# Kernel tuning notes

Measured on AMD Instinct MI355X. Metric: run time of the kernel, lower is better.

Reference implementation:

```python
import jax, jax.numpy as jnp
import numpy as np

B, S, N, FI = 16, 96, 128, 1
H_LSTM, NLAYERS = 128, 3
COMB = H_LSTM + 16 * N  # 128 + 16*128 = 2176


def setup_inputs() -> dict:
    key = jax.random.key(0)
    ks = list(jax.random.split(key, 24))
    def nrm(k, shape, scale=0.1):
        return jax.random.normal(k, shape, dtype=jnp.float32) * scale
    x = jax.random.normal(ks[0], (B, S, N, FI), dtype=jnp.float32)
    adj = jax.random.randint(ks[1], (N, N), 0, 2).astype(jnp.float32)
    adj = jnp.maximum(adj, jnp.eye(N, dtype=jnp.float32))  # self-loops so no row fully masked
    return {
        "x": x, "adj": adj,
        "W_emb": nrm(ks[2], (1, 32)), "b_emb": jnp.zeros((32,), jnp.float32),
        "W1": nrm(ks[3], (32, 32)), "a1": nrm(ks[4], (64,)),
        "W2": nrm(ks[5], (32, 16)), "a2": nrm(ks[6], (32,)),
        "lstm_Wih": nrm(ks[7], (NLAYERS, 4 * H_LSTM, N)),
        "lstm_Whh": nrm(ks[8], (NLAYERS, 4 * H_LSTM, H_LSTM)),
        "lstm_bih": jnp.zeros((NLAYERS, 4 * H_LSTM), jnp.float32),
        "lstm_bhh": jnp.zeros((NLAYERS, 4 * H_LSTM), jnp.float32),
        "head_W1": nrm(ks[9], (3, COMB, 64), 0.05), "head_b1": jnp.zeros((3, 64), jnp.float32),
        "head_W2": nrm(ks[10], (3, 64, 32)), "head_b2": jnp.zeros((3, 32), jnp.float32),
        "W3d": nrm(ks[11], (32, 1)), "b3d": jnp.zeros((1,), jnp.float32),
        "W3r": nrm(ks[12], (32, 1)), "b3r": jnp.zeros((1,), jnp.float32),
        "W3v": nrm(ks[13], (32, 2)), "b3v": jnp.zeros((2,), jnp.float32),
    }


def gat(h, adj, W, a, apply_elu):
    # h: [M, N, Fin]; equivalent to concat-matmul score: e_ij = leakyrelu(a_l.Wh_i + a_r.Wh_j)
    Wh = h @ W                      # [M, N, Fout]
    f = W.shape[1]
    left = Wh @ a[:f]               # [M, N]
    right = Wh @ a[f:]              # [M, N]
    e = jax.nn.leaky_relu(left[:, :, None] + right[:, None, :], 0.2)  # [M, N, N]
    e = jnp.where(adj[None, :, :] > 0, e, jnp.float32(-9e15))
    attn = jax.nn.softmax(e, axis=2)
    out = jnp.einsum('mij,mjf->mif', attn, Wh)
    return (jax.nn.elu(out) if apply_elu else out), attn


def _lstm_layer(seq, Wih, Whh, bih, bhh):
    # seq: [B, S, D]; PyTorch gate order i, f, g, o
    Bz, Hh = seq.shape[0], Whh.shape[1]
    b = bih + bhh
    def step(carry, xt):
        h, c = carry
        g = xt @ Wih.T + h @ Whh.T + b  # [B, 4H]
        i, f, gg, o = jnp.split(g, 4, axis=1)
        c = jax.nn.sigmoid(f) * c + jax.nn.sigmoid(i) * jnp.tanh(gg)
        h = jax.nn.sigmoid(o) * jnp.tanh(c)
        return (h, c), h
    init = (jnp.zeros((Bz, Hh), seq.dtype), jnp.zeros((Bz, Hh), seq.dtype))
    _, hs = jax.lax.scan(step, init, jnp.swapaxes(seq, 0, 1))
    return jnp.swapaxes(hs, 0, 1)


def lstm_forward(seq, Wih, Whh, bih, bhh):
    h = seq
    for l in range(Wih.shape[0]):  # 3 layers (inference: inter-layer dropout is identity)
        h = _lstm_layer(h, Wih[l], Whh[l], bih[l], bhh[l])
    return h


def reference(x, adj, W_emb, b_emb, W1, a1, W2, a2,
              lstm_Wih, lstm_Whh, lstm_bih, lstm_bhh,
              head_W1, head_b1, head_W2, head_b2,
              W3d, b3d, W3r, b3r, W3v, b3v):
    Bz, Sz, Nz, _ = x.shape
    x_emb = (x @ W_emb + b_emb).reshape(Bz * Sz, Nz, -1)  # [B*S, N, 32]
    xg, _ = gat(x_emb, adj, W1, a1, True)
    xg, attn2 = gat(xg, adj, W2, a2, False)
    xg_out = xg.reshape(Bz, Sz, -1)[:, -1, :]             # [B, 16*N]
    xl = lstm_forward(x.reshape(Bz, Sz, Nz), lstm_Wih, lstm_Whh, lstm_bih, lstm_bhh)
    xl_out = xl[:, -1, :]                                 # [B, 128]
    c = jnp.concatenate([xl_out, xg_out], axis=1)         # [B, COMB]
    h1 = jax.nn.relu(jnp.einsum('bc,kcd->kbd', c, head_W1) + head_b1[:, None, :])
    h2 = jax.nn.relu(jnp.einsum('kbd,kde->kbe', h1, head_W2) + head_b2[:, None, :])
    d = h2[0] @ W3d + b3d
    r = h2[1] @ W3r + b3r
    v = h2[2] @ W3v + b3v
    return (d, r, v, attn2)
```

## Files before the change

### kernel.cpp

```cpp
#include <hip/hip_runtime.h>
#include <hip/hip_bf16.h>


typedef _Float16 half8 __attribute__((ext_vector_type(8)));
typedef float floatx4 __attribute__((ext_vector_type(4)));
typedef float float4v __attribute__((ext_vector_type(4)));

#define LOG2E 1.44269504088896f

__device__ __forceinline__ float fast_exp(float x) {
    return __builtin_amdgcn_exp2f(x * LOG2E);
}
__device__ __forceinline__ float sigm(float x) {
    x = fminf(fmaxf(x, -30.f), 30.f);
    return __builtin_amdgcn_rcpf(1.f + __builtin_amdgcn_exp2f(-x * LOG2E));
}
__device__ __forceinline__ float tanhp(float x) {
    x = fminf(fmaxf(x, -15.f), 15.f);
    float e = __builtin_amdgcn_exp2f(-2.f * LOG2E * x);
    return (1.f - e) * __builtin_amdgcn_rcpf(1.f + e);
}
__device__ __forceinline__ void split8v(float4v v0, float4v v1, half8& hi, half8& lo) {
#pragma unroll
    for (int j = 0; j < 4; ++j) {
        _Float16 h = (_Float16)v0[j];
        hi[j] = h; lo[j] = (_Float16)(v0[j] - (float)h);
    }
#pragma unroll
    for (int j = 0; j < 4; ++j) {
        _Float16 h = (_Float16)v1[j];
        hi[4 + j] = h; lo[4 + j] = (_Float16)(v1[j] - (float)h);
    }
}

struct LstmSh {
    float hbuf[2][544];
    float stage[16 * 132];
};
struct GatSh {
    unsigned long long adjm[256];
    float xv[128];
    float u1[32], v1[32], coef[4];
    float s1v[128];
    float h2s[128 * 33];
    float wh2[128 * 17];
    float Lv[128], Rv[128], rd2[128];
    float d_h[4][128], s_h[4][128];
};
union ShU { LstmSh l; GatSh g; };

__device__ __forceinline__ void l0_body(LstmSh& sh, int b,
    const float* __restrict__ x, const float* __restrict__ Wih,
    const float* __restrict__ Whh, const float* __restrict__ bih,
    const float* __restrict__ bhh,
    float* __restrict__ Pre0,
    float* __restrict__ Hout,
    int* __restrict__ fHout)
{
    int tid = threadIdx.x;
    int w = tid >> 6, lane = tid & 63, quad = lane >> 4, sub = lane & 15;
    int hu = 16 * w + sub, c4 = quad;

    __builtin_amdgcn_s_setprio(1);
    {
        half8 bhi[4][4], blo[4][4];
        float bias[4];
#pragma unroll
        for (int tt = 0; tt < 4; ++tt) {
            int r = tt * 128 + 16 * w + sub;
            bias[tt] = bih[r] + bhh[r];
#pragma unroll
            for (int kc = 0; kc < 4; ++kc) {
                const float4v* p = (const float4v*)(Wih + r * 128 + kc * 32 + quad * 8);
                split8v(p[0], p[1], bhi[tt][kc], blo[tt][kc]);
            }
        }
        for (int mt = 0; mt < 6; ++mt) {
            half8 ahi[4], alo[4];
            const float* arow = x + b * 12288 + (mt * 16 + sub) * 128;
#pragma unroll
            for (int kc = 0; kc < 4; ++kc) {
                const float4v* p = (const float4v*)(arow + kc * 32 + quad * 8);
                split8v(p[0], p[1], ahi[kc], alo[kc]);
            }
            floatx4 acc[4];
#pragma unroll
            for (int tt = 0; tt < 4; ++tt) {
                floatx4 a = {bias[tt], bias[tt], bias[tt], bias[tt]};
                acc[tt] = a;
            }
#pragma unroll
            for (int tt = 0; tt < 4; ++tt)
#pragma unroll
                for (int kc = 0; kc < 4; ++kc) {
                    acc[tt] = __builtin_amdgcn_mfma_f32_16x16x32_f16(ahi[kc], bhi[tt][kc], acc[tt], 0, 0, 0);
                    acc[tt] = __builtin_amdgcn_mfma_f32_16x16x32_f16(ahi[kc], blo[tt][kc], acc[tt], 0, 0, 0);
                    acc[tt] = __builtin_amdgcn_mfma_f32_16x16x32_f16(alo[kc], bhi[tt][kc], acc[tt], 0, 0, 0);
                }
#pragma unroll
            for (int tt = 0; tt < 4; ++tt)
#pragma unroll
                for (int reg = 0; reg < 4; ++reg)
                    Pre0[(mt * 16 + quad * 4 + reg) * 512 + tt * 128 + 16 * w + sub] = acc[tt][reg];
        }
    }
    float4v wgt[4][8];
#pragma unroll
    for (int g = 0; g < 4; ++g) {
        const float4v* p = (const float4v*)(Whh + (g * 128 + hu) * 128 + c4 * 32);
#pragma unroll
        for (int k = 0; k < 8; ++k) wgt[g][k] = p[k];
    }
    sh.hbuf[0][c4 * 136 + hu] = 0.f;
    float cvar = 0.f;
    __syncthreads();

    for (int t = 0; t < 96; ++t) {
        int rb = t & 1, wb = rb ^ 1;
        float pre[4];
#pragma unroll
        for (int g = 0; g < 4; ++g)
            pre[g] = Pre0[t * 512 + g * 128 + hu];
        const float4v* hc = (const float4v*)(&sh.hbuf[rb][c4 * 168]);
        float4v p4[4];
#pragma unroll
        for (int g = 0; g < 4; ++g) { float4v z = {0.f,0.f,0.f,0.f}; p4[g] = z; }
#pragma unroll
        for (int k = 0; k < 8; ++k) {
            float4v hv = hc[k];
#pragma unroll
            for (int g = 0; g < 4; ++g) p4[g] += wgt[g][k] * hv;
        }
        float p[4];
#pragma unroll
        for (int g = 0; g < 4; ++g) {
            float s = p4[g].x + p4[g].y + p4[g].z + p4[g].w;
            s += __shfl_xor(s, 16, 64);
            s += __shfl_xor(s, 32, 64);
            p[g] = s + pre[g];
        }
        float c = sigm(p[1]) * cvar + sigm(p[0]) * tanhp(p[2]);
        cvar = c;
        float h = sigm(p[3]) * tanhp(c);
        sh.hbuf[wb][c4 * 136 + hu] = h;
        if (c4 == 0) sh.stage[(t & 15) * 132 + hu] = h;
        __syncthreads();
        if ((t & 15) == 15) {
            int k = t >> 4;
            float* outp = Hout + k * 2048;
#pragma unroll
            for (int u = 0; u < 4; ++u) {
                int e = tid * 4 + u;
                atomicExch(&outp[e], sh.stage[(e >> 7) * 132 + (e & 127)]);
            }
            __syncthreads();
            if (tid == 0) atomicExch(&fHout[k], 1);
        }
    }
    __builtin_amdgcn_s_setprio(0);
}

__device__ __forceinline__ void proj_body(LstmSh& sh, int layer,
    const float* __restrict__ Wih, const float* __restrict__ bih,
    const float* __restrict__ bhh,
    const float* __restrict__ Hin,
    int* __restrict__ fH,
    float* __restrict__ PreRing,
    int* __restrict__ fP,
    int* __restrict__ cons)
{
    int tid = threadIdx.x;
    int w = tid >> 6, lane = tid & 63, quad = lane >> 4, sub = lane & 15;
    const float* WihL = Wih + layer * 65536;

    half8 bhi[4][4], blo[4][4];
    float bias[4];
#pragma unroll
    for (int tt = 0; tt < 4; ++tt) {
        int r = tt * 128 + 16 * w + sub;
        bias[tt] = bih[layer * 512 + r] + bhh[layer * 512 + r];
#pragma unroll
        for (int kc = 0; kc < 4; ++kc) {
            const float4v* p = (const float4v*)(WihL + r * 128 + kc * 32 + quad * 8);
            split8v(p[0], p[1], bhi[tt][kc], blo[tt][kc]);
        }
    }
    for (int k = 0; k < 6; ++k) {
        if (tid == 0) {
            while (atomicAdd(&fH[k], 0) == 0) __builtin_amdgcn_s_sleep(16);
        }
        __syncthreads();
        {
            const float* inp = Hin + k * 2048;
#pragma unroll
            for (int u = 0; u < 4; ++u) {
                int e = tid * 4 + u;
                sh.stage[(e >> 7) * 132 + (e & 127)] =
                    atomicAdd((float*)&inp[e], 0.f);
            }
        }
        __syncthreads();
        half8 ahi[4], alo[4];
        const float* arow = &sh.stage[sub * 132];
#pragma unroll
        for (int kc = 0; kc < 4; ++kc) {
            const float4v* p = (const float4v*)(arow + kc * 32 + quad * 8);
            split8v(p[0], p[1], ahi[kc], alo[kc]);
        }
        floatx4 acc[4];
#pragma unroll
        for (int tt = 0; tt < 4; ++tt) {
            floatx4 a = {bias[tt], bias[tt], bias[tt], bias[tt]};
            acc[tt] = a;
        }
#pragma unroll
        for (int tt = 0; tt < 4; ++tt)
#pragma unroll
            for (int kc = 0; kc < 4; ++kc) {
                acc[tt] = __builtin_amdgcn_mfma_f32_16x16x32_f16(ahi[kc], bhi[tt][kc], acc[tt], 0, 0, 0);
                acc[tt] = __builtin_amdgcn_mfma_f32_16x16x32_f16(ahi[kc], blo[tt][kc], acc[tt], 0, 0, 0);
                acc[tt] = __builtin_amdgcn_mfma_f32_16x16x32_f16(alo[kc], bhi[tt][kc], acc[tt], 0, 0, 0);
            }
        if (k >= 3) {
            if (tid == 0) {
                while (atomicAdd(cons, 0) < k - 2) __builtin_amdgcn_s_sleep(16);
            }
            __syncthreads();
        }
        float* dst = PreRing + (k % 3) * 8192;
#pragma unroll
        for (int tt = 0; tt < 4; ++tt)
#pragma unroll
            for (int reg = 0; reg < 4; ++reg)
                dst[(quad * 4 + reg) * 512 + tt * 128 + 16 * w + sub] = acc[tt][reg];
        __syncthreads();
        if (tid == 0) {
            __threadfence();
            atomicExch(&fP[k], 1);
        }
    }
}

__device__ __forceinline__ void rec_body(LstmSh& sh, int b, int layer,
    const float* __restrict__ Whh,
    const float* __restrict__ PreRing, int* __restrict__ fP,
    int* __restrict__ cons,
    float* __restrict__ Hout, int* __restrict__ fHout,
    float* __restrict__ xl_out)
{
    int tid = threadIdx.x;
    int w = tid >> 6, lane = tid & 63, quad = lane >> 4, sub = lane & 15;
    int hu = 16 * w + sub, c4 = quad;
    const float* WhhL = Whh + layer * 65536;

    __builtin_amdgcn_s_setprio(1);
    float4v wgt[4][8];
#pragma unroll
    for (int g = 0; g < 4; ++g) {
        const float4v* p = (const float4v*)(WhhL + (g * 128 + hu) * 128 + c4 * 32);
#pragma unroll
        for (int k = 0; k < 8; ++k) wgt[g][k] = p[k];
    }
    sh.hbuf[0][c4 * 136 + hu] = 0.f;
    float cvar = 0.f;
    __syncthreads();

    for (int k = 0; k < 6; ++k) {
        if (tid == 0) {
            while (atomicAdd(&fP[k], 0) == 0) __builtin_amdgcn_s_sleep(16);
            __threadfence();
        }
        __syncthreads();
        const float* PreC = PreRing + (k % 3) * 8192;
        for (int tl = 0; tl < 16; ++tl) {
            int t = k * 16 + tl;
            int rb = t & 1, wb = rb ^ 1;
            float pre[4];
#pragma unroll
            for (int g = 0; g < 4; ++g)
                pre[g] = PreC[tl * 512 + g * 128 + hu];
            const float4v* hc = (const float4v*)(&sh.hbuf[rb][c4 * 168]);
            float4v p4[4];
#pragma unroll
            for (int g = 0; g < 4; ++g) { float4v z = {0.f,0.f,0.f,0.f}; p4[g] = z; }
#pragma unroll
            for (int kk = 0; kk < 8; ++kk) {
                float4v hv = hc[kk];
#pragma unroll
                for (int g = 0; g < 4; ++g) p4[g] += wgt[g][kk] * hv;
            }
            float p[4];
#pragma unroll
            for (int g = 0; g < 4; ++g) {
                float s = p4[g].x + p4[g].y + p4[g].z + p4[g].w;
                s += __shfl_xor(s, 16, 64);
                s += __shfl_xor(s, 32, 64);
                p[g] = s + pre[g];
            }
            float c = sigm(p[1]) * cvar + sigm(p[0]) * tanhp(p[2]);
            cvar = c;
            float h = sigm(p[3]) * tanhp(c);
            sh.hbuf[wb][c4 * 136 + hu] = h;
            if (c4 == 0) {
                if (layer == 1) sh.stage[tl * 132 + hu] = h;
                else if (t == 95) xl_out[b * 128 + hu] = h;
            }
            __syncthreads();
        }
        if (tid == 0) atomicExch(cons, k + 1);
        if (layer == 1) {
            float* outp = Hout + k * 2048;
#pragma unroll
            for (int u = 0; u < 4; ++u) {
                int e = tid * 4 + u;
                atomicExch(&outp[e], sh.stage[(e >> 7) * 132 + (e & 127)]);
            }
            __syncthreads();
            if (tid == 0) atomicExch(&fHout[k], 1);
        }
    }
    __builtin_amdgcn_s_setprio(0);
}

__device__ __forceinline__ void gat_body(GatSh& s, int m,
    const float* __restrict__ x, const float* __restrict__ adj,
    const float* __restrict__ W_emb, const float* __restrict__ b_emb,
    const float* __restrict__ W1, const float* __restrict__ a1,
    const float* __restrict__ W2, const float* __restrict__ a2,
    float* __restrict__ attn_out, float* __restrict__ xg)
{
    int tid = threadIdx.x;

    if (tid < 128) s.xv[tid] = x[m * 128 + tid];
#pragma unroll
    for (int base = 0; base < 16384; base += 512) {
        int idx = base + tid;
        unsigned long long msk = __ballot(adj[idx] > 0.f);
        if ((tid & 63) == 0) s.adjm[idx >> 6] = msk;
    }
    if (tid < 32) {
        float su = 0.f, sv = 0.f;
        for (int kk = 0; kk < 32; ++kk) {
            float w1v = W1[kk * 32 + tid];
            su += W_emb[kk] * w1v;
            sv += b_emb[kk] * w1v;
        }
        s.u1[tid] = su; s.v1[tid] = sv;
    }
    __syncthreads();
    if (tid < 4) {
        const float* av = a1 + ((tid >= 2) ? 32 : 0);
        const float* uv = (tid & 1) ? s.v1 : s.u1;
        float sum = 0.f;
        for (int f = 0; f < 32; ++f) sum += uv[f] * av[f];
        s.coef[tid] = sum;
    }
    __syncthreads();
    float cL = s.coef[0], dL = s.coef[1], cR = s.coef[2], dR = s.coef[3];

    {
        int i = tid & 127, q = tid >> 7;
        unsigned int ms = (unsigned int)(s.adjm[(i << 1) | (q >> 1)] >> ((q & 1) * 32));
        float Li = s.xv[i] * cL + dL;
        float den = 0.f, wsum = 0.f;
        int j0 = q * 32;
#pragma unroll
        for (int jj = 0; jj < 32; ++jj) {
            if ((ms >> jj) & 1) {
                float xj = s.xv[j0 + jj];
                float e = Li + xj * cR + dR;
                e = e > 0.f ? e : 0.2f * e;
                float p = fast_exp(e);
                den += p; wsum += p * xj;
            }
        }
        s.d_h[q][i] = den; s.s_h[q][i] = wsum;
    }
    __syncthreads();
    if (tid < 128) {
        float den = 0.f, wsum = 0.f;
#pragma unroll
        for (int q = 0; q < 4; ++q) { den += s.d_h[q][tid]; wsum += s.s_h[q][tid]; }
        s.s1v[tid] = wsum / den;
    }
    __syncthreads();
#pragma unroll
    for (int e0 = 0; e0 < 4096; e0 += 512) {
        int e = e0 + tid;
        int i = e >> 5, f = e & 31;
        float v = s.s1v[i] * s.u1[f] + s.v1[f];
        s.h2s[i * 33 + f] = v > 0.f ? v : fast_exp(v) - 1.f;
    }
    __syncthreads();
    {
        int i = tid >> 2, g0 = (tid & 3) * 4;
        float accv[4] = {0.f, 0.f, 0.f, 0.f};
        for (int f = 0; f < 32; ++f) {
            float hv = s.h2s[i * 33 + f];
#pragma unroll
            for (int g = 0; g < 4; ++g) accv[g] += hv * W2[f * 16 + g0 + g];
        }
#pragma unroll
        for (int g = 0; g < 4; ++g) s.wh2[i * 17 + g0 + g] = accv[g];
    }
    __syncthreads();
    if (tid < 256) {
        int i = tid & 127, which = tid >> 7;
        const float* aa = a2 + which * 16;
        float sum = 0.f;
#pragma unroll
        for (int g = 0; g < 16; ++g) sum += s.wh2[i * 17 + g] * aa[g];
        (which ? s.Rv : s.Lv)[i] = sum;
    }
    __syncthreads();
    {
        int i = tid & 127, q = tid >> 7;
        unsigned int ms = (unsigned int)(s.adjm[(i << 1) | (q >> 1)] >> ((q & 1) * 32));
        float Li = s.Lv[i];
        float den = 0.f;
        int j0 = q * 32;
#pragma unroll
        for (int jj = 0; jj < 32; ++jj) {
            if ((ms >> jj) & 1) {
                float e = Li + s.Rv[j0 + jj];
                e = e > 0.f ? e : 0.2f * e;
                den += fast_exp(e);
            }
        }
        s.d_h[q][i] = den;
    }
    __syncthreads();
    if (tid < 128) {
        float den = 0.f;
#pragma unroll
        for (int q = 0; q < 4; ++q) den += s.d_h[q][tid];
        s.rd2[tid] = 1.0f / den;
    }
    __syncthreads();

    float* aout = attn_out + (size_t)m * 16384;
#pragma unroll
    for (int k = 0; k < 8; ++k) {
        int e0 = k * 2048 + tid * 4;
        int i = e0 >> 7, j0 = e0 & 127;
        unsigned int bits = (unsigned int)(s.adjm[(i << 1) | (j0 >> 6)] >> (j0 & 63)) & 0xFu;
        float Li = s.Lv[i], ri = s.rd2[i];
        float4v p;
#pragma unroll
        for (int u = 0; u < 4; ++u) {
            float pv = 0.f;
            if ((bits >> u) & 1) {
                float e = Li + s.Rv[j0 + u];
                e = e > 0.f ? e : 0.2f * e;
                pv = fast_exp(e) * ri;
            }
            p[u] = pv;
        }
        *(float4v*)(aout + e0) = p;
    }

    if (m % 96 == 95) {
        int b = m / 96;
        int i = tid >> 2, g0 = (tid & 3) * 4;
        unsigned long long mA = s.adjm[i << 1], mB = s.adjm[(i << 1) | 1];
        float Li = s.Lv[i], ri = s.rd2[i];
        float accv[4] = {0.f, 0.f, 0.f, 0.f};
        for (int j = 0; j < 128; ++j) {
            unsigned long long mm = (j < 64) ? mA : mB;
            if ((mm >> (j & 63)) & 1) {
                float e = Li + s.Rv[j];
                e = e > 0.f ? e : 0.2f * e;
                float p = fast_exp(e) * ri;
#pragma unroll
                for (int g = 0; g < 4; ++g) accv[g] += p * s.wh2[j * 17 + g0 + g];
            }
        }
#pragma unroll
        for (int g = 0; g < 4; ++g) xg[b * 2048 + i * 16 + g0 + g] = accv[g];
    }
}

__global__ __launch_bounds__(512, 2) void fused_kernel(
    const float* __restrict__ x, const float* __restrict__ adj,
    const float* __restrict__ W_emb, const float* __restrict__ b_emb,
    const float* __restrict__ W1, const float* __restrict__ a1,
    const float* __restrict__ W2, const float* __restrict__ a2,
    const float* __restrict__ Wih, const float* __restrict__ Whh,
    const float* __restrict__ bih, const float* __restrict__ bhh,
    float* __restrict__ Pre0, float* __restrict__ Pre1, float* __restrict__ Pre2,
    float* __restrict__ H0, float* __restrict__ H1,
    int* __restrict__ flags, float* __restrict__ xl_out,
    float* __restrict__ attn_out, float* __restrict__ xg)
{
    __shared__ ShU sh;
    int bb = blockIdx.x;
    if (bb < 80) {
        int grp = bb >> 4, b = bb & 15;
        int* F = flags + b * 32;
        if (grp == 0) {
            l0_body(sh.l, b, x, Wih, Whh, bih, bhh,
                    Pre0 + b * 49152, H0 + b * 12288, F + 0);
        } else if (grp == 1) {
            proj_body(sh.l, 1, Wih, bih, bhh,
                      H0 + b * 12288, F + 0, Pre1 + b * 24576, F + 8, F + 14);
        } else if (grp == 2) {
            rec_body(sh.l, b, 1, Whh,
                     Pre1 + b * 24576, F + 8, F + 14,
                     H1 + b * 12288, F + 16, nullptr);
        } else if (grp == 3) {
            proj_body(sh.l, 2, Wih, bih, bhh,
                      H1 + b * 12288, F + 16, Pre2 + b * 24576, F + 24, F + 30);
        } else {
            rec_body(sh.l, b, 2, Whh,
                     Pre2 + b * 24576, F + 24, F + 30,
                     nullptr, nullptr, xl_out);
        }
    } else {
        gat_body(sh.g, bb - 80, x, adj, W_emb, b_emb, W1, a1, W2, a2, attn_out, xg);
    }
}

__global__ __launch_bounds__(256) void head_partial_kernel(
    const float* __restrict__ xl, const float* __restrict__ xg,
    const float* __restrict__ W1, float* __restrict__ hp)
{
    int k = blockIdx.x >> 4, chunk = blockIdx.x & 15;
    int d = threadIdx.x & 63, bg = threadIdx.x >> 6;
    float acc[4] = {0.f, 0.f, 0.f, 0.f};
    int c0 = chunk * 136;
    for (int cc = c0; cc < c0 + 136; ++cc) {
        float wv = W1[(k * 2176 + cc) * 64 + d];
#pragma unroll
        for (int u = 0; u < 4; ++u) {
            int b = bg * 4 + u;
            float cv = (cc < 128) ? xl[b * 128 + cc] : xg[b * 2048 + cc - 128];
            acc[u] += wv * cv;
        }
    }
#pragma unroll
    for (int u = 0; u < 4; ++u)
        hp[(((k * 16 + chunk) * 16) + bg * 4 + u) * 64 + d] = acc[u];
}

__global__ __launch_bounds__(256) void head_final_kernel(
    const float* __restrict__ hp, const float* __restrict__ b1,
    const float* __restrict__ W2, const float* __restrict__ b2,
    const float* __restrict__ W3d, const float* __restrict__ b3d,
    const float* __restrict__ W3r, const float* __restrict__ b3r,
    const float* __restrict__ W3v, const float* __restrict__ b3v,
    float* __restrict__ out)
{
    __shared__ float h1s[3 * 16 * 64];
    __shared__ float h2s[3 * 16 * 32];
    int tid = threadIdx.x;
    for (int o = tid; o < 3072; o += 256) {
        int k = o >> 10, rem = o & 1023, b = rem >> 6, d = rem & 63;
        float s = b1[k * 64 + d];
        for (int ch = 0; ch < 16; ++ch)
            s += hp[(((k * 16 + ch) * 16) + b) * 64 + d];
        h1s[o] = fmaxf(s, 0.f);
    }
    __syncthreads();
    for (int o = tid; o < 1536; o += 256) {
        int k = o >> 9, rem = o & 511, b = rem >> 5, e = rem & 31;
        float s = b2[k * 32 + e];
        for (int dd = 0; dd < 64; ++dd)
            s += h1s[(k * 16 + b) * 64 + dd] * W2[(k * 64 + dd) * 32 + e];
        h2s[o] = fmaxf(s, 0.f);
    }
    __syncthreads();
    if (tid < 64) {
        if (tid < 16) {
            int b = tid; float s = b3d[0];
            for (int e = 0; e < 32; ++e) s += h2s[b * 32 + e] * W3d[e];
            out[b] = s;
        } else if (tid < 32) {
            int b = tid - 16; float s = b3r[0];
            for (int e = 0; e < 32; ++e) s += h2s[(16 + b) * 32 + e] * W3r[e];
            out[16 + b] = s;
        } else {
            int b = (tid - 32) >> 1, j = tid & 1; float s = b3v[j];
            for (int e = 0; e < 32; ++e) s += h2s[(32 + b) * 32 + e] * W3v[e * 2 + j];
            out[32 + b * 2 + j] = s;
        }
    }
}

extern "C" void kernel_launch(void* const* d_in, const int* in_sizes, int n_in,
                              void* d_out, int out_size, void* d_ws, size_t ws_size,
                              hipStream_t stream)
{
    const float* x     = (const float*)d_in[0];
    const float* adj   = (const float*)d_in[1];
    const float* W_emb = (const float*)d_in[2];
    const float* b_emb = (const float*)d_in[3];
    const float* W1    = (const float*)d_in[4];
    const float* a1    = (const float*)d_in[5];
    const float* W2    = (const float*)d_in[6];
    const float* a2    = (const float*)d_in[7];
    const float* Wih   = (const float*)d_in[8];
    const float* Whh   = (const float*)d_in[9];
    const float* bih   = (const float*)d_in[10];
    const float* bhh   = (const float*)d_in[11];
    const float* hW1   = (const float*)d_in[12];
    const float* hb1   = (const float*)d_in[13];
    const float* hW2   = (const float*)d_in[14];
    const float* hb2   = (const float*)d_in[15];
    const float* W3d   = (const float*)d_in[16];
    const float* b3d   = (const float*)d_in[17];
    const float* W3r   = (const float*)d_in[18];
    const float* b3r   = (const float*)d_in[19];
    const float* W3v   = (const float*)d_in[20];
    const float* b3v   = (const float*)d_in[21];

    float* out = (float*)d_out;
    float* wsf = (float*)d_ws;
    float* XG    = wsf;
    float* XL    = wsf + 32768;
    float* HP    = wsf + 34816;
    int*   FLAGS = (int*)(wsf + 83968);
    float* PRE0  = wsf + 84992;
    float* PRE1  = wsf + 871424;
    float* PRE2  = wsf + 1264640;
    float* H0    = wsf + 1657856;
    float* H1    = wsf + 1854464;

    hipMemsetAsync(FLAGS, 0, 16 * 32 * sizeof(int), stream);
    fused_kernel<<<1616, 512, 0, stream>>>(
        x, adj, W_emb, b_emb, W1, a1, W2, a2,
        Wih, Whh, bih, bhh, PRE0, PRE1, PRE2, H0, H1, FLAGS, XL, out + 64, XG);
    head_partial_kernel<<<48, 256, 0, stream>>>(XL, XG, hW1, HP);
    head_final_kernel<<<1, 256, 0, stream>>>(HP, hb1, hW2, hb2, W3d, b3d, W3r, b3r, W3v, b3v, out);
}
```

Before: 353.1 us.

## Double-buffer layer-0 staging, tighten spin sleeps, fuse head kernels via last-block counter

Layer-0 recurrence now double-buffers its output stage so it no longer needs an extra barrier before raising the chunk flag; each flag is raised one step later, and the last one after the loop. Spin-wait sleeps drop from 16 to 2 and the projection workers get raised wave priority. The two head kernels merge into one launch where the last block to finish, found through an atomic counter, does the reduction and the final layers. This trims launch overhead and handoff latency along the LSTM pipeline, at the cost of more polling traffic and a one-step delay on the layer-0 flags.

```diff
diff --git a/kernel.cpp b/kernel.cpp
--- a/kernel.cpp
+++ b/kernel.cpp
@@ -35,7 +35,7 @@
 
 struct LstmSh {
     float hbuf[2][544];
-    float stage[16 * 132];
+    float stage[2][16 * 132];
 };
 struct GatSh {
     unsigned long long adjm[256];
@@ -143,36 +143,38 @@
         cvar = c;
         float h = sigm(p[3]) * tanhp(c);
         sh.hbuf[wb][c4 * 136 + hu] = h;
-        if (c4 == 0) sh.stage[(t & 15) * 132 + hu] = h;
+        if (c4 == 0) sh.stage[(t >> 4) & 1][(t & 15) * 132 + hu] = h;
         __syncthreads();
         if ((t & 15) == 15) {
             int k = t >> 4;
             float* outp = Hout + k * 2048;
+            const float* st = sh.stage[k & 1];
 #pragma unroll
             for (int u = 0; u < 4; ++u) {
                 int e = tid * 4 + u;
-                atomicExch(&outp[e], sh.stage[(e >> 7) * 132 + (e & 127)]);
-            }
-            __syncthreads();
-            if (tid == 0) atomicExch(&fHout[k], 1);
-        }
-    }
+                atomicExch(&outp[e], st[(e >> 7) * 132 + (e & 127)]);
+            }
+        } else if ((t & 15) == 0 && t >= 16 && tid == 0) {
+            atomicExch(&fHout[(t >> 4) - 1], 1);
+        }
+    }
+    __syncthreads();
+    if (tid == 0) atomicExch(&fHout[5], 1);
     __builtin_amdgcn_s_setprio(0);
 }
 
 __device__ __forceinline__ void proj_body(LstmSh& sh, int layer,
     const float* __restrict__ Wih, const float* __restrict__ bih,
     const float* __restrict__ bhh,
-    const float* __restrict__ Hin,
-    int* __restrict__ fH,
-    float* __restrict__ PreRing,
-    int* __restrict__ fP,
+    const float* __restrict__ Hin, int* __restrict__ fH,
+    float* __restrict__ PreRing, int* __restrict__ fP,
     int* __restrict__ cons)
 {
     int tid = threadIdx.x;
     int w = tid >> 6, lane = tid & 63, quad = lane >> 4, sub = lane & 15;
     const float* WihL = Wih + layer * 65536;
 
+    __builtin_amdgcn_s_setprio(1);
     half8 bhi[4][4], blo[4][4];
     float bias[4];
 #pragma unroll
@@ -187,7 +189,7 @@
     }
     for (int k = 0; k < 6; ++k) {
         if (tid == 0) {
-            while (atomicAdd(&fH[k], 0) == 0) __builtin_amdgcn_s_sleep(16);
+            while (atomicAdd(&fH[k], 0) == 0) __builtin_amdgcn_s_sleep(2);
         }
         __syncthreads();
         {
@@ -195,13 +197,13 @@
 #pragma unroll
             for (int u = 0; u < 4; ++u) {
                 int e = tid * 4 + u;
-                sh.stage[(e >> 7) * 132 + (e & 127)] =
+                sh.stage[0][(e >> 7) * 132 + (e & 127)] =
                     atomicAdd((float*)&inp[e], 0.f);
             }
         }
         __syncthreads();
         half8 ahi[4], alo[4];
-        const float* arow = &sh.stage[sub * 132];
+        const float* arow = &sh.stage[0][sub * 132];
 #pragma unroll
         for (int kc = 0; kc < 4; ++kc) {
             const float4v* p = (const float4v*)(arow + kc * 32 + quad * 8);
@@ -223,7 +225,7 @@
             }
         if (k >= 3) {
             if (tid == 0) {
-                while (atomicAdd(cons, 0) < k - 2) __builtin_amdgcn_s_sleep(16);
+                while (atomicAdd(cons, 0) < k - 2) __builtin_amdgcn_s_sleep(2);
             }
             __syncthreads();
         }
@@ -239,6 +241,7 @@
             atomicExch(&fP[k], 1);
         }
     }
+    __builtin_amdgcn_s_setprio(0);
 }
 
 __device__ __forceinline__ void rec_body(LstmSh& sh, int b, int layer,
@@ -267,7 +270,7 @@
 
     for (int k = 0; k < 6; ++k) {
         if (tid == 0) {
-            while (atomicAdd(&fP[k], 0) == 0) __builtin_amdgcn_s_sleep(16);
+            while (atomicAdd(&fP[k], 0) == 0) __builtin_amdgcn_s_sleep(2);
             __threadfence();
         }
         __syncthreads();
@@ -302,7 +305,7 @@
             float h = sigm(p[3]) * tanhp(c);
             sh.hbuf[wb][c4 * 136 + hu] = h;
             if (c4 == 0) {
-                if (layer == 1) sh.stage[tl * 132 + hu] = h;
+                if (layer == 1) sh.stage[0][tl * 132 + hu] = h;
                 else if (t == 95) xl_out[b * 128 + hu] = h;
             }
             __syncthreads();
@@ -313,7 +316,7 @@
 #pragma unroll
             for (int u = 0; u < 4; ++u) {
                 int e = tid * 4 + u;
-                atomicExch(&outp[e], sh.stage[(e >> 7) * 132 + (e & 127)]);
+                atomicExch(&outp[e], sh.stage[0][(e >> 7) * 132 + (e & 127)]);
             }
             __syncthreads();
             if (tid == 0) atomicExch(&fHout[k], 1);
@@ -520,30 +523,11 @@
     }
 }
 
-__global__ __launch_bounds__(256) void head_partial_kernel(
+__global__ __launch_bounds__(256) void head_kernel(
     const float* __restrict__ xl, const float* __restrict__ xg,
-    const float* __restrict__ W1, float* __restrict__ hp)
-{
-    int k = blockIdx.x >> 4, chunk = blockIdx.x & 15;
-    int d = threadIdx.x & 63, bg = threadIdx.x >> 6;
-    float acc[4] = {0.f, 0.f, 0.f, 0.f};
-    int c0 = chunk * 136;
-    for (int cc = c0; cc < c0 + 136; ++cc) {
-        float wv = W1[(k * 2176 + cc) * 64 + d];
-#pragma unroll
-        for (int u = 0; u < 4; ++u) {
-            int b = bg * 4 + u;
-            float cv = (cc < 128) ? xl[b * 128 + cc] : xg[b * 2048 + cc - 128];
-            acc[u] += wv * cv;
-        }
-    }
-#pragma unroll
-    for (int u = 0; u < 4; ++u)
-        hp[(((k * 16 + chunk) * 16) + bg * 4 + u) * 64 + d] = acc[u];
-}
-
-__global__ __launch_bounds__(256) void head_final_kernel(
-    const float* __restrict__ hp, const float* __restrict__ b1,
+    const float* __restrict__ W1, float* __restrict__ hp,
+    int* __restrict__ counter,
+    const float* __restrict__ b1,
     const float* __restrict__ W2, const float* __restrict__ b2,
     const float* __restrict__ W3d, const float* __restrict__ b3d,
     const float* __restrict__ W3r, const float* __restrict__ b3r,
@@ -552,7 +536,35 @@
 {
     __shared__ float h1s[3 * 16 * 64];
     __shared__ float h2s[3 * 16 * 32];
+    __shared__ int isLast;
     int tid = threadIdx.x;
+    {
+        int k = blockIdx.x >> 4, chunk = blockIdx.x & 15;
+        int d = tid & 63, bg = tid >> 6;
+        float acc[4] = {0.f, 0.f, 0.f, 0.f};
+        int c0 = chunk * 136;
+        for (int cc = c0; cc < c0 + 136; ++cc) {
+            float wv = W1[(k * 2176 + cc) * 64 + d];
+#pragma unroll
+            for (int u = 0; u < 4; ++u) {
+                int b = bg * 4 + u;
+                float cv = (cc < 128) ? xl[b * 128 + cc] : xg[b * 2048 + cc - 128];
+                acc[u] += wv * cv;
+            }
+        }
+#pragma unroll
+        for (int u = 0; u < 4; ++u)
+            hp[(((k * 16 + chunk) * 16) + bg * 4 + u) * 64 + d] = acc[u];
+    }
+    __threadfence();
+    if (tid == 0) {
+        int old = atomicAdd(counter, 1);
+        isLast = (old == 47);
+    }
+    __syncthreads();
+    if (!isLast) return;
+    __threadfence();
+
     for (int o = tid; o < 3072; o += 256) {
         int k = o >> 10, rem = o & 1023, b = rem >> 6, d = rem & 63;
         float s = b1[k * 64 + d];
@@ -625,10 +637,11 @@
     float* H0    = wsf + 1657856;
     float* H1    = wsf + 1854464;
 
-    hipMemsetAsync(FLAGS, 0, 16 * 32 * sizeof(int), stream);
+    hipMemsetAsync(FLAGS, 0, (16 * 32 + 8) * sizeof(int), stream);
     fused_kernel<<<1616, 512, 0, stream>>>(
         x, adj, W_emb, b_emb, W1, a1, W2, a2,
         Wih, Whh, bih, bhh, PRE0, PRE1, PRE2, H0, H1, FLAGS, XL, out + 64, XG);
-    head_partial_kernel<<<48, 256, 0, stream>>>(XL, XG, hW1, HP);
-    head_final_kernel<<<1, 256, 0, stream>>>(HP, hb1, hW2, hb2, W3d, b3d, W3r, b3r, W3v, b3v, out);
-}
+    head_kernel<<<48, 256, 0, stream>>>(
+        XL, XG, hW1, HP, FLAGS + 512,
+        hb1, hW2, hb2, W3d, b3d, W3r, b3r, W3v, b3v, out);
+}
```

Result: slower. 360.9 us (+2.2%).

## Batch LSTM recurrence across all sequences into one MFMA block per layer

Applied to the files above, without the earlier changes.

Replaces the per-batch-element recurrent blocks (16 per layer, scalar FMA dot products with shuffles) with a single block per layer that handles all 16 batch rows together. It computes h@Whh^T with split-fp16 MFMA and stores preactivations in a batch-interleaved layout. Projection blocks now run per batch element and signal per-(chunk, batch) flags, and layer 0 gets a separate projection stage. Spin-wait sleeps are shortened and launch bounds drop to one block per SM. The serial chain now depends on one block and 16-way flag polling, and the lower occupancy may slow the concurrent GAT blocks.

```diff
diff --git a/kernel.cpp b/kernel.cpp
--- a/kernel.cpp
+++ b/kernel.cpp
@@ -33,11 +33,14 @@
     }
 }
 
-struct LstmSh {
-    float hbuf[2][544];
+struct __align__(16) MegaSh {
+    float g[512 * 20];
+    float h[16 * 132];
+};
+struct __align__(16) ProjSh {
     float stage[16 * 132];
 };
-struct GatSh {
+struct __align__(16) GatSh {
     unsigned long long adjm[256];
     float xv[128];
     float u1[32], v1[32], coef[4];
@@ -47,132 +50,79 @@
     float Lv[128], Rv[128], rd2[128];
     float d_h[4][128], s_h[4][128];
 };
-union ShU { LstmSh l; GatSh g; };
-
-__device__ __forceinline__ void l0_body(LstmSh& sh, int b,
+union ShU { MegaSh m; ProjSh p; GatSh gt; };
+
+__device__ __forceinline__ void l0proj_body(int b,
     const float* __restrict__ x, const float* __restrict__ Wih,
-    const float* __restrict__ Whh, const float* __restrict__ bih,
-    const float* __restrict__ bhh,
-    float* __restrict__ Pre0,
-    float* __restrict__ Hout,
-    int* __restrict__ fHout)
+    const float* __restrict__ bih, const float* __restrict__ bhh,
+    float* __restrict__ PreM0, int* __restrict__ fL0)
 {
     int tid = threadIdx.x;
     int w = tid >> 6, lane = tid & 63, quad = lane >> 4, sub = lane & 15;
-    int hu = 16 * w + sub, c4 = quad;
 
     __builtin_amdgcn_s_setprio(1);
-    {
-        half8 bhi[4][4], blo[4][4];
-        float bias[4];
+    half8 bhi[4][4], blo[4][4];
+    float bias[4];
+#pragma unroll
+    for (int tt = 0; tt < 4; ++tt) {
+        int r = tt * 128 + 16 * w + sub;
+        bias[tt] = bih[r] + bhh[r];
+#pragma unroll
+        for (int kc = 0; kc < 4; ++kc) {
+            const float4v* p = (const float4v*)(Wih + r * 128 + kc * 32 + quad * 8);
+            split8v(p[0], p[1], bhi[tt][kc], blo[tt][kc]);
+        }
+    }
+    for (int mt = 0; mt < 6; ++mt) {
+        half8 ahi[4], alo[4];
+        const float* arow = x + b * 12288 + (mt * 16 + sub) * 128;
+#pragma unroll
+        for (int kc = 0; kc < 4; ++kc) {
+            const float4v* p = (const float4v*)(arow + kc * 32 + quad * 8);
+            split8v(p[0], p[1], ahi[kc], alo[kc]);
+        }
+        floatx4 acc[4];
 #pragma unroll
         for (int tt = 0; tt < 4; ++tt) {
-            int r = tt * 128 + 16 * w + sub;
-            bias[tt] = bih[r] + bhh[r];
+            floatx4 a = {bias[tt], bias[tt], bias[tt], bias[tt]};
+            acc[tt] = a;
+        }
+#pragma unroll
+        for (int tt = 0; tt < 4; ++tt)
 #pragma unroll
             for (int kc = 0; kc < 4; ++kc) {
-                const float4v* p = (const float4v*)(Wih + r * 128 + kc * 32 + quad * 8);
-                split8v(p[0], p[1], bhi[tt][kc], blo[tt][kc]);
-            }
-        }
-        for (int mt = 0; mt < 6; ++mt) {
-            half8 ahi[4], alo[4];
-            const float* arow = x + b * 12288 + (mt * 16 + sub) * 128;
-#pragma unroll
-            for (int kc = 0; kc < 4; ++kc) {
-                const float4v* p = (const float4v*)(arow + kc * 32 + quad * 8);
-                split8v(p[0], p[1], ahi[kc], alo[kc]);
-            }
-            floatx4 acc[4];
-#pragma unroll
-            for (int tt = 0; tt < 4; ++tt) {
-                floatx4 a = {bias[tt], bias[tt], bias[tt], bias[tt]};
-                acc[tt] = a;
-            }
-#pragma unroll
-            for (int tt = 0; tt < 4; ++tt)
-#pragma unroll
-                for (int kc = 0; kc < 4; ++kc) {
-                    acc[tt] = __builtin_amdgcn_mfma_f32_16x16x32_f16(ahi[kc], bhi[tt][kc], acc[tt], 0, 0, 0);
-                    acc[tt] = __builtin_amdgcn_mfma_f32_16x16x32_f16(ahi[kc], blo[tt][kc], acc[tt], 0, 0, 0);
-                    acc[tt] = __builtin_amdgcn_mfma_f32_16x16x32_f16(alo[kc], bhi[tt][kc], acc[tt], 0, 0, 0);
-                }
-#pragma unroll
-            for (int tt = 0; tt < 4; ++tt)
-#pragma unroll
-                for (int reg = 0; reg < 4; ++reg)
-                    Pre0[(mt * 16 + quad * 4 + reg) * 512 + tt * 128 + 16 * w + sub] = acc[tt][reg];
-        }
-    }
-    float4v wgt[4][8];
-#pragma unroll
-    for (int g = 0; g < 4; ++g) {
-        const float4v* p = (const float4v*)(Whh + (g * 128 + hu) * 128 + c4 * 32);
-#pragma unroll
-        for (int k = 0; k < 8; ++k) wgt[g][k] = p[k];
-    }
-    sh.hbuf[0][c4 * 136 + hu] = 0.f;
-    float cvar = 0.f;
-    __syncthreads();
-
-    for (int t = 0; t < 96; ++t) {
-        int rb = t & 1, wb = rb ^ 1;
-        float pre[4];
-#pragma unroll
-        for (int g = 0; g < 4; ++g)
-            pre[g] = Pre0[t * 512 + g * 128 + hu];
-        const float4v* hc = (const float4v*)(&sh.hbuf[rb][c4 * 168]);
-        float4v p4[4];
-#pragma unroll
-        for (int g = 0; g < 4; ++g) { float4v z = {0.f,0.f,0.f,0.f}; p4[g] = z; }
-#pragma unroll
-        for (int k = 0; k < 8; ++k) {
-            float4v hv = hc[k];
-#pragma unroll
-            for (int g = 0; g < 4; ++g) p4[g] += wgt[g][k] * hv;
-        }
-        float p[4];
-#pragma unroll
-        for (int g = 0; g < 4; ++g) {
-            float s = p4[g].x + p4[g].y + p4[g].z + p4[g].w;
-            s += __shfl_xor(s, 16, 64);
-            s += __shfl_xor(s, 32, 64);
-            p[g] = s + pre[g];
-        }
-        float c = sigm(p[1]) * cvar + sigm(p[0]) * tanhp(p[2]);
-        cvar = c;
-        float h = sigm(p[3]) * tanhp(c);
-        sh.hbuf[wb][c4 * 136 + hu] = h;
-        if (c4 == 0) sh.stage[(t & 15) * 132 + hu] = h;
+                acc[tt] = __builtin_amdgcn_mfma_f32_16x16x32_f16(ahi[kc], bhi[tt][kc], acc[tt], 0, 0, 0);
+                acc[tt] = __builtin_amdgcn_mfma_f32_16x16x32_f16(ahi[kc], blo[tt][kc], acc[tt], 0, 0, 0);
+                acc[tt] = __builtin_amdgcn_mfma_f32_16x16x32_f16(alo[kc], bhi[tt][kc], acc[tt], 0, 0, 0);
+            }
+#pragma unroll
+        for (int tt = 0; tt < 4; ++tt) {
+            int r2 = tt * 128 + 16 * w + sub;
+#pragma unroll
+            for (int reg = 0; reg < 4; ++reg)
+                PreM0[(((mt * 16 + quad * 4 + reg) * 512) + r2) * 16 + b] = acc[tt][reg];
+        }
         __syncthreads();
-        if ((t & 15) == 15) {
-            int k = t >> 4;
-            float* outp = Hout + k * 2048;
-#pragma unroll
-            for (int u = 0; u < 4; ++u) {
-                int e = tid * 4 + u;
-                atomicExch(&outp[e], sh.stage[(e >> 7) * 132 + (e & 127)]);
-            }
-            __syncthreads();
-            if (tid == 0) atomicExch(&fHout[k], 1);
+        if (tid == 0) {
+            __threadfence();
+            atomicExch(&fL0[b * 8 + mt], 1);
         }
     }
     __builtin_amdgcn_s_setprio(0);
 }
 
-__device__ __forceinline__ void proj_body(LstmSh& sh, int layer,
+__device__ __forceinline__ void proj_body(ProjSh& sh, int layer, int b,
     const float* __restrict__ Wih, const float* __restrict__ bih,
     const float* __restrict__ bhh,
-    const float* __restrict__ Hin,
-    int* __restrict__ fH,
-    float* __restrict__ PreRing,
-    int* __restrict__ fP,
+    const float* __restrict__ Hin, int* __restrict__ fH,
+    float* __restrict__ PreRing, int* __restrict__ fP,
     int* __restrict__ cons)
 {
     int tid = threadIdx.x;
     int w = tid >> 6, lane = tid & 63, quad = lane >> 4, sub = lane & 15;
     const float* WihL = Wih + layer * 65536;
 
+    __builtin_amdgcn_s_setprio(1);
     half8 bhi[4][4], blo[4][4];
     float bias[4];
 #pragma unroll
@@ -187,7 +137,7 @@
     }
     for (int k = 0; k < 6; ++k) {
         if (tid == 0) {
-            while (atomicAdd(&fH[k], 0) == 0) __builtin_amdgcn_s_sleep(16);
+            while (atomicAdd(&fH[k], 0) == 0) __builtin_amdgcn_s_sleep(2);
         }
         __syncthreads();
         {
@@ -223,100 +173,134 @@
             }
         if (k >= 3) {
             if (tid == 0) {
-                while (atomicAdd(cons, 0) < k - 2) __builtin_amdgcn_s_sleep(16);
+                while (atomicAdd(cons, 0) < k - 2) __builtin_amdgcn_s_sleep(2);
             }
             __syncthreads();
         }
-        float* dst = PreRing + (k % 3) * 8192;
-#pragma unroll
-        for (int tt = 0; tt < 4; ++tt)
+        float* dst = PreRing + (k % 3) * 131072;
+#pragma unroll
+        for (int tt = 0; tt < 4; ++tt) {
+            int r2 = tt * 128 + 16 * w + sub;
 #pragma unroll
             for (int reg = 0; reg < 4; ++reg)
-                dst[(quad * 4 + reg) * 512 + tt * 128 + 16 * w + sub] = acc[tt][reg];
+                dst[(((quad * 4 + reg) * 512) + r2) * 16 + b] = acc[tt][reg];
+        }
         __syncthreads();
         if (tid == 0) {
             __threadfence();
-            atomicExch(&fP[k], 1);
-        }
-    }
-}
-
-__device__ __forceinline__ void rec_body(LstmSh& sh, int b, int layer,
-    const float* __restrict__ Whh,
-    const float* __restrict__ PreRing, int* __restrict__ fP,
+            atomicExch(&fP[k * 16 + b], 1);
+        }
+    }
+    __builtin_amdgcn_s_setprio(0);
+}
+
+__device__ __forceinline__ void megarec_body(MegaSh& sh, int layer,
+    const float* __restrict__ WhhL,
+    const float* __restrict__ PreSrc,
+    int* __restrict__ fPre,
     int* __restrict__ cons,
-    float* __restrict__ Hout, int* __restrict__ fHout,
+    float* __restrict__ Hout,
+    int* __restrict__ fHout,
     float* __restrict__ xl_out)
 {
     int tid = threadIdx.x;
     int w = tid >> 6, lane = tid & 63, quad = lane >> 4, sub = lane & 15;
-    int hu = 16 * w + sub, c4 = quad;
-    const float* WhhL = Whh + layer * 65536;
+    int bb = tid >> 5, u0 = (tid & 31) * 4;
 
     __builtin_amdgcn_s_setprio(1);
-    float4v wgt[4][8];
-#pragma unroll
-    for (int g = 0; g < 4; ++g) {
-        const float4v* p = (const float4v*)(WhhL + (g * 128 + hu) * 128 + c4 * 32);
-#pragma unroll
-        for (int k = 0; k < 8; ++k) wgt[g][k] = p[k];
-    }
-    sh.hbuf[0][c4 * 136 + hu] = 0.f;
-    float cvar = 0.f;
-    __syncthreads();
-
+    half8 bhi[4][4], blo[4][4];
+#pragma unroll
+    for (int nt = 0; nt < 4; ++nt) {
+        int rB = w * 64 + nt * 16 + sub;
+#pragma unroll
+        for (int kc = 0; kc < 4; ++kc) {
+            const float4v* p = (const float4v*)(WhhL + rB * 128 + kc * 32 + quad * 8);
+            split8v(p[0], p[1], bhi[nt][kc], blo[nt][kc]);
+        }
+    }
+    {
+        float4v z = {0.f, 0.f, 0.f, 0.f};
+        *(float4v*)&sh.h[bb * 132 + u0] = z;
+    }
+    float cvar[4] = {0.f, 0.f, 0.f, 0.f};
+    __syncthreads();
+
+    float4v pren[4];
     for (int k = 0; k < 6; ++k) {
         if (tid == 0) {
-            while (atomicAdd(&fP[k], 0) == 0) __builtin_amdgcn_s_sleep(16);
+            if (layer == 0) {
+                for (int b2 = 0; b2 < 16; ++b2)
+                    while (atomicAdd(&fPre[b2 * 8 + k], 0) == 0) __builtin_amdgcn_s_sleep(2);
+            } else {
+                for (int b2 = 0; b2 < 16; ++b2)
+                    while (atomicAdd(&fPre[k * 16 + b2], 0) == 0) __builtin_amdgcn_s_sleep(2);
+            }
             __threadfence();
         }
         __syncthreads();
-        const float* PreC = PreRing + (k % 3) * 8192;
+        const float* PreC = (layer == 0) ? PreSrc + k * (16 * 8192)
+                                         : PreSrc + (k % 3) * 131072;
         for (int tl = 0; tl < 16; ++tl) {
             int t = k * 16 + tl;
-            int rb = t & 1, wb = rb ^ 1;
-            float pre[4];
-#pragma unroll
-            for (int g = 0; g < 4; ++g)
-                pre[g] = PreC[tl * 512 + g * 128 + hu];
-            const float4v* hc = (const float4v*)(&sh.hbuf[rb][c4 * 168]);
-            float4v p4[4];
-#pragma unroll
-            for (int g = 0; g < 4; ++g) { float4v z = {0.f,0.f,0.f,0.f}; p4[g] = z; }
-#pragma unroll
-            for (int kk = 0; kk < 8; ++kk) {
-                float4v hv = hc[kk];
-#pragma unroll
-                for (int g = 0; g < 4; ++g) p4[g] += wgt[g][kk] * hv;
-            }
-            float p[4];
-#pragma unroll
-            for (int g = 0; g < 4; ++g) {
-                float s = p4[g].x + p4[g].y + p4[g].z + p4[g].w;
-                s += __shfl_xor(s, 16, 64);
-                s += __shfl_xor(s, 32, 64);
-                p[g] = s + pre[g];
-            }
-            float c = sigm(p[1]) * cvar + sigm(p[0]) * tanhp(p[2]);
-            cvar = c;
-            float h = sigm(p[3]) * tanhp(c);
-            sh.hbuf[wb][c4 * 136 + hu] = h;
-            if (c4 == 0) {
-                if (layer == 1) sh.stage[tl * 132 + hu] = h;
-                else if (t == 95) xl_out[b * 128 + hu] = h;
-            }
+            float4v acc[4];
+            if (tl == 0) {
+#pragma unroll
+                for (int nt = 0; nt < 4; ++nt)
+                    acc[nt] = *(const float4v*)(PreC + ((0 * 512) + (w * 64 + nt * 16 + sub)) * 16 + quad * 4);
+            } else {
+#pragma unroll
+                for (int nt = 0; nt < 4; ++nt) acc[nt] = pren[nt];
+            }
+            if (tl < 15) {
+#pragma unroll
+                for (int nt = 0; nt < 4; ++nt)
+                    pren[nt] = *(const float4v*)(PreC + (((tl + 1) * 512) + (w * 64 + nt * 16 + sub)) * 16 + quad * 4);
+            }
+            half8 ahi[4], alo[4];
+#pragma unroll
+            for (int kc = 0; kc < 4; ++kc) {
+                const float4v* p = (const float4v*)(&sh.h[sub * 132 + kc * 32 + quad * 8]);
+                split8v(p[0], p[1], ahi[kc], alo[kc]);
+            }
+#pragma unroll
+            for (int kc = 0; kc < 4; ++kc)
+#pragma unroll
+                for (int nt = 0; nt < 4; ++nt) {
+                    acc[nt] = __builtin_amdgcn_mfma_f32_16x16x32_f16(ahi[kc], bhi[nt][kc], acc[nt], 0, 0, 0);
+                    acc[nt] = __builtin_amdgcn_mfma_f32_16x16x32_f16(ahi[kc], blo[nt][kc], acc[nt], 0, 0, 0);
+                    acc[nt] = __builtin_amdgcn_mfma_f32_16x16x32_f16(alo[kc], bhi[nt][kc], acc[nt], 0, 0, 0);
+                }
+#pragma unroll
+            for (int nt = 0; nt < 4; ++nt)
+                *(float4v*)&sh.g[(w * 64 + nt * 16 + sub) * 20 + quad * 4] = acc[nt];
             __syncthreads();
-        }
-        if (tid == 0) atomicExch(cons, k + 1);
-        if (layer == 1) {
-            float* outp = Hout + k * 2048;
-#pragma unroll
-            for (int u = 0; u < 4; ++u) {
-                int e = tid * 4 + u;
-                atomicExch(&outp[e], sh.stage[(e >> 7) * 132 + (e & 127)]);
+            float hr[4];
+#pragma unroll
+            for (int j = 0; j < 4; ++j) {
+                int u = u0 + j;
+                float gi = sh.g[u * 20 + bb];
+                float gf = sh.g[(128 + u) * 20 + bb];
+                float gg = sh.g[(256 + u) * 20 + bb];
+                float go = sh.g[(384 + u) * 20 + bb];
+                float c = sigm(gf) * cvar[j] + sigm(gi) * tanhp(gg);
+                cvar[j] = c;
+                hr[j] = sigm(go) * tanhp(c);
+            }
+            float4v hv = {hr[0], hr[1], hr[2], hr[3]};
+            *(float4v*)&sh.h[bb * 132 + u0] = hv;
+            if (layer < 2) {
+                *(float4v*)(Hout + bb * 12288 + t * 128 + u0) = hv;
+            } else if (t == 95) {
+                *(float4v*)(xl_out + bb * 128 + u0) = hv;
             }
             __syncthreads();
-            if (tid == 0) atomicExch(&fHout[k], 1);
+        }
+        if (tid == 0) {
+            if (layer > 0) atomicExch(cons, k + 1);
+            if (layer < 2) {
+                __threadfence();
+                atomicExch(&fHout[k], 1);
+            }
         }
     }
     __builtin_amdgcn_s_setprio(0);
@@ -480,43 +464,41 @@
     }
 }
 
-__global__ __launch_bounds__(512, 2) void fused_kernel(
+__global__ __launch_bounds__(512, 1) void fused_kernel(
     const float* __restrict__ x, const float* __restrict__ adj,
     const float* __restrict__ W_emb, const float* __restrict__ b_emb,
     const float* __restrict__ W1, const float* __restrict__ a1,
     const float* __restrict__ W2, const float* __restrict__ a2,
     const float* __restrict__ Wih, const float* __restrict__ Whh,
     const float* __restrict__ bih, const float* __restrict__ bhh,
-    float* __restrict__ Pre0, float* __restrict__ Pre1, float* __restrict__ Pre2,
+    float* __restrict__ PreM0, float* __restrict__ Ring1, float* __restrict__ Ring2,
     float* __restrict__ H0, float* __restrict__ H1,
     int* __restrict__ flags, float* __restrict__ xl_out,
     float* __restrict__ attn_out, float* __restrict__ xg)
 {
     __shared__ ShU sh;
     int bb = blockIdx.x;
-    if (bb < 80) {
-        int grp = bb >> 4, b = bb & 15;
-        int* F = flags + b * 32;
-        if (grp == 0) {
-            l0_body(sh.l, b, x, Wih, Whh, bih, bhh,
-                    Pre0 + b * 49152, H0 + b * 12288, F + 0);
-        } else if (grp == 1) {
-            proj_body(sh.l, 1, Wih, bih, bhh,
-                      H0 + b * 12288, F + 0, Pre1 + b * 24576, F + 8, F + 14);
-        } else if (grp == 2) {
-            rec_body(sh.l, b, 1, Whh,
-                     Pre1 + b * 24576, F + 8, F + 14,
-                     H1 + b * 12288, F + 16, nullptr);
-        } else if (grp == 3) {
-            proj_body(sh.l, 2, Wih, bih, bhh,
-                      H1 + b * 12288, F + 16, Pre2 + b * 24576, F + 24, F + 30);
-        } else {
-            rec_body(sh.l, b, 2, Whh,
-                     Pre2 + b * 24576, F + 24, F + 30,
+    if (bb < 16) {
+        l0proj_body(bb, x, Wih, bih, bhh, PreM0, flags + 0);
+    } else if (bb == 16) {
+        megarec_body(sh.m, 0, Whh, PreM0, flags + 0, nullptr,
+                     H0, flags + 248, nullptr);
+    } else if (bb < 33) {
+        proj_body(sh.p, 1, bb - 17, Wih, bih, bhh,
+                  H0 + (bb - 17) * 12288, flags + 248,
+                  Ring1, flags + 128, flags + 240);
+    } else if (bb == 33) {
+        megarec_body(sh.m, 1, Whh + 65536, Ring1, flags + 128, flags + 240,
+                     H1, flags + 408, nullptr);
+    } else if (bb < 50) {
+        proj_body(sh.p, 2, bb - 34, Wih, bih, bhh,
+                  H1 + (bb - 34) * 12288, flags + 408,
+                  Ring2, flags + 288, flags + 400);
+    } else if (bb == 50) {
+        megarec_body(sh.m, 2, Whh + 131072, Ring2, flags + 288, flags + 400,
                      nullptr, nullptr, xl_out);
-        }
     } else {
-        gat_body(sh.g, bb - 80, x, adj, W_emb, b_emb, W1, a1, W2, a2, attn_out, xg);
+        gat_body(sh.gt, bb - 51, x, adj, W_emb, b_emb, W1, a1, W2, a2, attn_out, xg);
     }
 }
 
@@ -619,16 +601,16 @@
     float* XL    = wsf + 32768;
     float* HP    = wsf + 34816;
     int*   FLAGS = (int*)(wsf + 83968);
-    float* PRE0  = wsf + 84992;
-    float* PRE1  = wsf + 871424;
-    float* PRE2  = wsf + 1264640;
-    float* H0    = wsf + 1657856;
-    float* H1    = wsf + 1854464;
-
-    hipMemsetAsync(FLAGS, 0, 16 * 32 * sizeof(int), stream);
-    fused_kernel<<<1616, 512, 0, stream>>>(
+    float* PREM0 = wsf + 84480;
+    float* RING1 = wsf + 870912;
+    float* RING2 = wsf + 1264128;
+    float* H0    = wsf + 1657344;
+    float* H1    = wsf + 1853952;
+
+    hipMemsetAsync(FLAGS, 0, 512 * sizeof(int), stream);
+    fused_kernel<<<1587, 512, 0, stream>>>(
         x, adj, W_emb, b_emb, W1, a1, W2, a2,
-        Wih, Whh, bih, bhh, PRE0, PRE1, PRE2, H0, H1, FLAGS, XL, out + 64, XG);
+        Wih, Whh, bih, bhh, PREM0, RING1, RING2, H0, H1, FLAGS, XL, out + 64, XG);
     head_partial_kernel<<<48, 256, 0, stream>>>(XL, XG, hW1, HP);
     head_final_kernel<<<1, 256, 0, stream>>>(HP, hb1, hW2, hb2, W3d, b3d, W3r, b3r, W3v, b3v, out);
 }
```

Result: slower. 644.9 us (+82.6%).
